# Optimization experiments

Measured on AMD Instinct MI355X. Metric: run time of the kernel, lower is better.

## Reference

```python
import jax, jax.numpy as jnp
import numpy as np

BASE = 64
EOS = 0
PAD = BASE + 1      # 65
BOS = BASE + 2      # 66
VOCAB = BASE + 3    # 67 (use_bos=True)
NACT = BASE + 1     # 65
H = 512
MAX_LEN = 20
BATCH = 32768


def setup_inputs() -> dict:
    key = jax.random.key(0)
    ks = jax.random.split(key, 12)
    s = 1.0 / np.sqrt(H)  # torch-like init scale, avoids gate saturation
    emb = jax.random.normal(ks[1], (VOCAB, H), jnp.float32) * s
    emb = emb.at[PAD].set(0.0)  # padding_idx row is zero in nn.Embedding
    return {
        'encoded': jax.random.normal(ks[0], (BATCH, H), jnp.float32),
        'emb': emb,
        'W_ih': jax.random.normal(ks[2], (4 * H, H), jnp.float32) * s,
        'W_hh': jax.random.normal(ks[3], (4 * H, H), jnp.float32) * s,
        'b_ih': jax.random.normal(ks[4], (4 * H,), jnp.float32) * s,
        'b_hh': jax.random.normal(ks[5], (4 * H,), jnp.float32) * s,
        'Wc': jax.random.normal(ks[6], (H, H), jnp.float32) * s,
        'bc': jax.random.normal(ks[7], (H,), jnp.float32) * s,
        'Wh': jax.random.normal(ks[8], (H, H), jnp.float32) * s,
        'bh': jax.random.normal(ks[9], (H,), jnp.float32) * s,
        'Wa': jax.random.normal(ks[10], (NACT, H), jnp.float32) * s,
        'ba': jax.random.normal(ks[11], (NACT,), jnp.float32) * s,
    }


def _decode(encoded, emb, W_ih, W_hh, b_ih, b_hh, Wc, bc, Wh, bh, Wa, ba):
    B = encoded.shape[0]
    # NOTE: original passes (cell, hidden) to nn.LSTM, which reads it as (h0, c0).
    h0 = encoded @ Wc.T + bc  # cell_proj output -> used as h0
    c0 = encoded @ Wh.T + bh  # hidden_proj output -> used as c0
    last0 = jnp.full((B,), BOS, jnp.int32)
    stopped0 = jnp.zeros((B,), bool)

    def step(carry, _):
        h, c, last, stopped = carry
        x = emb[last]                                   # [B, H]
        gates = x @ W_ih.T + b_ih + h @ W_hh.T + b_hh   # [B, 4H]
        i, f, g, o = jnp.split(gates, 4, axis=-1)
        c = jax.nn.sigmoid(f) * c + jax.nn.sigmoid(i) * jnp.tanh(g)
        h = jax.nn.sigmoid(o) * jnp.tanh(c)
        logits = h @ Wa.T + ba                          # [B, NACT]
        logp = jax.nn.log_softmax(logits, axis=-1)
        action = jnp.argmax(logits, axis=-1).astype(jnp.int32)  # eval-mode greedy
        alive = (~stopped).astype(logits.dtype)
        ent = -jnp.sum(jnp.exp(logp) * logp, axis=-1) * alive
        lp = jnp.take_along_axis(logp, action[:, None], axis=-1)[:, 0] * alive
        action = jnp.where(stopped, PAD, action)
        stopped = stopped | (action == EOS)
        return (h, c, action, stopped), (action, lp, ent)

    _, (msg, lps, ents) = jax.lax.scan(step, (h0, c0, last0, stopped0), None, length=MAX_LEN)
    message = msg.T                                   # [B, L]
    log_probs = lps.T                                 # [B, L]
    entropy_steps = ents.T                            # [B, L]
    message_len = jnp.sum(message != PAD, axis=1, keepdims=True)  # [B, 1]
    entropy = jnp.sum(entropy_steps, axis=1, keepdims=True) / message_len.astype(entropy_steps.dtype)
    return entropy, log_probs, message, message_len


def reference(encoded, emb, W_ih, W_hh, b_ih, b_hh, Wc, bc, Wh, bh, Wa, ba):
    return _decode(encoded, emb, W_ih, W_hh, b_ih, b_hh, Wc, bc, Wh, bh, Wa, ba)
```

## Files before the change

kernel.cpp:

```cpp
#include <hip/hip_runtime.h>
#include <cmath>


#define HH      512
#define G4      2048
#define NACTS   65
#define NVOCAB  67
#define MAXLEN  20
#define NB      32768
#define TM      16
#define NTH     256
#define EOS_TOK 0
#define PAD_TOK 65
#define BOS_TOK 66
#define HSTR    516

__global__ void prep_gxa_kernel(const float* __restrict__ emb,
                                const float* __restrict__ W_ih,
                                const float* __restrict__ b_ih,
                                const float* __restrict__ b_hh,
                                float* __restrict__ gxa4) {
  int id = blockIdx.x * blockDim.x + threadIdx.x;
  if (id >= NVOCAB * G4) return;
  int a = id / G4, rem = id - a * G4;
  int t = rem >> 2, gate = rem & 3;
  int c = gate * HH + t;
  const float* e = emb + (size_t)a * HH;
  const float* w = W_ih + (size_t)c * HH;
  float acc = 0.f;
  for (int k = 0; k < HH; ++k) acc = fmaf(e[k], w[k], acc);
  gxa4[id] = acc + b_ih[c] + b_hh[c];
}

__global__ void prep_w4_kernel(const float* __restrict__ src,
                               float* __restrict__ dst, int cols) {
  int id = blockIdx.x * blockDim.x + threadIdx.x;
  if (id >= cols * HH) return;
  int k4 = id / (cols * 4);
  int rem = id - k4 * cols * 4;
  int c = rem >> 2, j = rem & 3;
  dst[id] = src[(size_t)c * HH + k4 * 4 + j];
}

__global__ void ws_sentinel_kernel(float* out) {
  out[threadIdx.x] = 123000.f;
}

#define FMA4(acc, h, wv) \
  acc = fmaf((h).x, (wv).x, fmaf((h).y, (wv).y, fmaf((h).z, (wv).z, fmaf((h).w, (wv).w, (acc)))))

__global__ __launch_bounds__(NTH, 2)
void decode_kernel(const float* __restrict__ encoded,
                   const float* __restrict__ gxa4,
                   const float* __restrict__ whh4,
                   const float* __restrict__ wc4,
                   const float* __restrict__ wh4,
                   const float* __restrict__ bc,
                   const float* __restrict__ bh,
                   const float* __restrict__ Wa,
                   const float* __restrict__ ba,
                   float* __restrict__ out) {
  __shared__ float sh_h[TM][HSTR];
  __shared__ float sh_wa[16][HSTR];
  __shared__ float sh_logits[TM][NACTS + 3];
  __shared__ int   sh_last[TM];
  __shared__ int   sh_stop[TM];
  __shared__ float sh_ent[TM];
  __shared__ int   sh_len[TM];

  const int t = threadIdx.x;
  const int row0 = blockIdx.x * TM;

  #pragma unroll
  for (int i = 0; i < (TM * HH / 4) / NTH; ++i) {
    int f4 = i * NTH + t;
    int idx = f4 * 4;
    int r = idx >> 9;
    int c = idx & (HH - 1);
    *reinterpret_cast<float4*>(&sh_h[r][c]) =
        *reinterpret_cast<const float4*>(encoded + (size_t)(row0 + r) * HH + c);
  }
  if (t < TM) { sh_last[t] = BOS_TOK; sh_stop[t] = 0; sh_ent[t] = 0.f; sh_len[t] = 0; }
  __syncthreads();

  float hacc[2][TM], cacc[2][TM];
  #pragma unroll
  for (int j = 0; j < 2; ++j)
    #pragma unroll
    for (int r = 0; r < TM; ++r) { hacc[j][r] = 0.f; cacc[j][r] = 0.f; }
  #pragma unroll 1
  for (int k4 = 0; k4 < HH / 4; ++k4) {
    const float* wcb = wc4 + ((size_t)k4 * HH + t) * 4;
    const float* whb = wh4 + ((size_t)k4 * HH + t) * 4;
    float4 wc0 = *reinterpret_cast<const float4*>(wcb);
    float4 wc1 = *reinterpret_cast<const float4*>(wcb + 1024);
    float4 wh0 = *reinterpret_cast<const float4*>(whb);
    float4 wh1 = *reinterpret_cast<const float4*>(whb + 1024);
    #pragma unroll
    for (int r = 0; r < TM; ++r) {
      float4 e = *reinterpret_cast<const float4*>(&sh_h[r][k4 * 4]);
      FMA4(hacc[0][r], e, wc0);
      FMA4(hacc[1][r], e, wc1);
      FMA4(cacc[0][r], e, wh0);
      FMA4(cacc[1][r], e, wh1);
    }
  }
  __syncthreads();
  float cst[2][TM];
  {
    float bc0 = bc[t], bc1 = bc[t + 256];
    float bh0 = bh[t], bh1 = bh[t + 256];
    #pragma unroll
    for (int r = 0; r < TM; ++r) {
      sh_h[r][t] = hacc[0][r] + bc0;
      sh_h[r][t + 256] = hacc[1][r] + bc1;
      cst[0][r] = cacc[0][r] + bh0;
      cst[1][r] = cacc[1][r] + bh1;
    }
  }
  __syncthreads();

  for (int step = 0; step < MAXLEN; ++step) {
    float ai[2][TM], af[2][TM], ag[2][TM], ao[2][TM];
    #pragma unroll
    for (int r = 0; r < TM; ++r) {
      const float* g0 = gxa4 + ((size_t)sh_last[r] * HH + t) * 4;
      float4 ga = *reinterpret_cast<const float4*>(g0);
      float4 gb = *reinterpret_cast<const float4*>(g0 + 1024);
      ai[0][r] = ga.x; af[0][r] = ga.y; ag[0][r] = ga.z; ao[0][r] = ga.w;
      ai[1][r] = gb.x; af[1][r] = gb.y; ag[1][r] = gb.z; ao[1][r] = gb.w;
    }
    #pragma unroll 1
    for (int k4 = 0; k4 < HH / 4; ++k4) {
      const float* wb = whh4 + (size_t)k4 * (G4 * 4) + t * 4;
      float4 wi0 = *reinterpret_cast<const float4*>(wb);
      float4 wf0 = *reinterpret_cast<const float4*>(wb + 2048);
      float4 wg0 = *reinterpret_cast<const float4*>(wb + 4096);
      float4 wo0 = *reinterpret_cast<const float4*>(wb + 6144);
      float4 wi1 = *reinterpret_cast<const float4*>(wb + 1024);
      float4 wf1 = *reinterpret_cast<const float4*>(wb + 2048 + 1024);
      float4 wg1 = *reinterpret_cast<const float4*>(wb + 4096 + 1024);
      float4 wo1 = *reinterpret_cast<const float4*>(wb + 6144 + 1024);
      #pragma unroll
      for (int r = 0; r < TM; ++r) {
        float4 h4 = *reinterpret_cast<const float4*>(&sh_h[r][k4 * 4]);
        FMA4(ai[0][r], h4, wi0);
        FMA4(af[0][r], h4, wf0);
        FMA4(ag[0][r], h4, wg0);
        FMA4(ao[0][r], h4, wo0);
        FMA4(ai[1][r], h4, wi1);
        FMA4(af[1][r], h4, wf1);
        FMA4(ag[1][r], h4, wg1);
        FMA4(ao[1][r], h4, wo1);
      }
    }
    __syncthreads();

    #pragma unroll
    for (int j = 0; j < 2; ++j) {
      int col = t + j * 256;
      #pragma unroll
      for (int r = 0; r < TM; ++r) {
        float iv = 1.f / (1.f + expf(-ai[j][r]));
        float fv = 1.f / (1.f + expf(-af[j][r]));
        float gv = tanhf(ag[j][r]);
        float ov = 1.f / (1.f + expf(-ao[j][r]));
        float cn = fmaf(fv, cst[j][r], iv * gv);
        cst[j][r] = cn;
        sh_h[r][col] = ov * tanhf(cn);
      }
    }
    __syncthreads();

    const int r_lg = t >> 4;
    const int a_lg = t & 15;
    for (int ab = 0; ab < 5; ++ab) {
      int a0 = ab * 16;
      int arows = (a0 + 16 <= NACTS) ? 16 : (NACTS - a0);
      int total4 = arows * HH / 4;
      for (int f4 = t; f4 < total4; f4 += NTH) {
        int idx = f4 * 4;
        int rr = idx >> 9;
        int cc = idx & (HH - 1);
        *reinterpret_cast<float4*>(&sh_wa[rr][cc]) =
            *reinterpret_cast<const float4*>(Wa + (size_t)(a0 + rr) * HH + cc);
      }
      __syncthreads();
      if (a_lg < arows) {
        float acc = 0.f;
        #pragma unroll 1
        for (int k4 = 0; k4 < HH / 4; ++k4) {
          float4 h4 = *reinterpret_cast<const float4*>(&sh_h[r_lg][k4 * 4]);
          float4 w4 = *reinterpret_cast<const float4*>(&sh_wa[a_lg][k4 * 4]);
          FMA4(acc, h4, w4);
        }
        sh_logits[r_lg][a0 + a_lg] = acc + ba[a0 + a_lg];
      }
      __syncthreads();
    }

    if (t < TM) {
      const int r = t;
      float m = sh_logits[r][0];
      int am = 0;
      #pragma unroll 1
      for (int a = 1; a < NACTS; ++a) {
        float v = sh_logits[r][a];
        if (v > m) { m = v; am = a; }
      }
      float s = 0.f;
      #pragma unroll 1
      for (int a = 0; a < NACTS; ++a) s += expf(sh_logits[r][a] - m);
      float logZ = m + logf(s);
      float pl = 0.f;
      #pragma unroll 1
      for (int a = 0; a < NACTS; ++a) {
        float l = sh_logits[r][a];
        pl = fmaf(expf(l - logZ), l, pl);
      }
      float ent = logZ - pl;
      int stopped = sh_stop[r];
      float lp   = stopped ? 0.f : (sh_logits[r][am] - logZ);
      float entc = stopped ? 0.f : ent;
      int act = stopped ? PAD_TOK : am;
      int grow = row0 + r;
      out[NB + (size_t)grow * MAXLEN + step] = lp;
      out[NB + (size_t)NB * MAXLEN + (size_t)grow * MAXLEN + step] = (float)act;
      sh_ent[r] += entc;
      if (act != PAD_TOK) sh_len[r] += 1;
      if (act == EOS_TOK) sh_stop[r] = 1;
      sh_last[r] = act;
    }
    __syncthreads();
  }

  if (t < TM) {
    int r = t, grow = row0 + r;
    float lenf = (float)sh_len[r];
    out[grow] = sh_ent[r] / lenf;
    out[NB + 2 * (size_t)NB * MAXLEN + grow] = lenf;
  }
}

extern "C" void kernel_launch(void* const* d_in, const int* in_sizes, int n_in,
                              void* d_out, int out_size, void* d_ws, size_t ws_size,
                              hipStream_t stream) {
  const float* encoded = (const float*)d_in[0];
  const float* emb     = (const float*)d_in[1];
  const float* W_ih    = (const float*)d_in[2];
  const float* W_hh    = (const float*)d_in[3];
  const float* b_ih    = (const float*)d_in[4];
  const float* b_hh    = (const float*)d_in[5];
  const float* Wc      = (const float*)d_in[6];
  const float* bc      = (const float*)d_in[7];
  const float* Wh      = (const float*)d_in[8];
  const float* bh      = (const float*)d_in[9];
  const float* Wa      = (const float*)d_in[10];
  const float* ba      = (const float*)d_in[11];
  float* out = (float*)d_out;

  size_t need = ((size_t)NVOCAB * G4 + (size_t)G4 * HH + 2 * (size_t)HH * HH) * 4;
  if (ws_size < need) {
    ws_sentinel_kernel<<<1, 64, 0, stream>>>(out);
    return;
  }

  float* ws   = (float*)d_ws;
  float* gxa4 = ws;
  float* whh4 = gxa4 + NVOCAB * G4;
  float* wc4  = whh4 + (size_t)HH * G4;
  float* wh4  = wc4 + (size_t)HH * HH;

  prep_gxa_kernel<<<(NVOCAB * G4 + 255) / 256, 256, 0, stream>>>(emb, W_ih, b_ih, b_hh, gxa4);
  prep_w4_kernel<<<(G4 * HH + 255) / 256, 256, 0, stream>>>(W_hh, whh4, G4);
  prep_w4_kernel<<<(HH * HH + 255) / 256, 256, 0, stream>>>(Wc, wc4, HH);
  prep_w4_kernel<<<(HH * HH + 255) / 256, 256, 0, stream>>>(Wh, wh4, HH);

  decode_kernel<<<NB / TM, NTH, 0, stream>>>(encoded, gxa4, whh4, wc4, wh4,
                                             bc, bh, Wa, ba, out);
}
```

Before: 21.04 ms.

## Read action-head weights from a padded interleaved global layout instead of staging through LDS

```diff
diff --git a/kernel.cpp b/kernel.cpp
--- a/kernel.cpp
+++ b/kernel.cpp
@@ -5,6 +5,7 @@
 #define HH      512
 #define G4      2048
 #define NACTS   65
+#define NAP     80
 #define NVOCAB  67
 #define MAXLEN  20
 #define NB      32768
@@ -42,6 +43,16 @@
   dst[id] = src[(size_t)c * HH + k4 * 4 + j];
 }
 
+__global__ void prep_wa4_kernel(const float* __restrict__ Wa,
+                                float* __restrict__ dst) {
+  int id = blockIdx.x * blockDim.x + threadIdx.x;
+  if (id >= (HH / 4) * NAP * 4) return;
+  int k4 = id / (NAP * 4);
+  int rem = id - k4 * NAP * 4;
+  int a = rem >> 2, j = rem & 3;
+  dst[id] = (a < NACTS) ? Wa[(size_t)a * HH + k4 * 4 + j] : 0.f;
+}
+
 __global__ void ws_sentinel_kernel(float* out) {
   out[threadIdx.x] = 123000.f;
 }
@@ -49,7 +60,7 @@
 #define FMA4(acc, h, wv) \
   acc = fmaf((h).x, (wv).x, fmaf((h).y, (wv).y, fmaf((h).z, (wv).z, fmaf((h).w, (wv).w, (acc)))))
 
-__global__ __launch_bounds__(NTH, 2)
+__global__ __launch_bounds__(NTH, 1)
 void decode_kernel(const float* __restrict__ encoded,
                    const float* __restrict__ gxa4,
                    const float* __restrict__ whh4,
@@ -57,11 +68,10 @@
                    const float* __restrict__ wh4,
                    const float* __restrict__ bc,
                    const float* __restrict__ bh,
-                   const float* __restrict__ Wa,
+                   const float* __restrict__ wa4,
                    const float* __restrict__ ba,
                    float* __restrict__ out) {
   __shared__ float sh_h[TM][HSTR];
-  __shared__ float sh_wa[16][HSTR];
   __shared__ float sh_logits[TM][NACTS + 3];
   __shared__ int   sh_last[TM];
   __shared__ int   sh_stop[TM];
@@ -172,32 +182,23 @@
     }
     __syncthreads();
 
-    const int r_lg = t >> 4;
-    const int a_lg = t & 15;
-    for (int ab = 0; ab < 5; ++ab) {
-      int a0 = ab * 16;
-      int arows = (a0 + 16 <= NACTS) ? 16 : (NACTS - a0);
-      int total4 = arows * HH / 4;
-      for (int f4 = t; f4 < total4; f4 += NTH) {
-        int idx = f4 * 4;
-        int rr = idx >> 9;
-        int cc = idx & (HH - 1);
-        *reinterpret_cast<float4*>(&sh_wa[rr][cc]) =
-            *reinterpret_cast<const float4*>(Wa + (size_t)(a0 + rr) * HH + cc);
-      }
-      __syncthreads();
-      if (a_lg < arows) {
+    {
+      const int r_lg = t >> 4;
+      const int a_lg = t & 15;
+      #pragma unroll 1
+      for (int ab = 0; ab < 5; ++ab) {
+        int a = ab * 16 + a_lg;
         float acc = 0.f;
-        #pragma unroll 1
+        #pragma unroll 4
         for (int k4 = 0; k4 < HH / 4; ++k4) {
           float4 h4 = *reinterpret_cast<const float4*>(&sh_h[r_lg][k4 * 4]);
-          float4 w4 = *reinterpret_cast<const float4*>(&sh_wa[a_lg][k4 * 4]);
+          float4 w4 = *reinterpret_cast<const float4*>(wa4 + ((size_t)k4 * NAP + a) * 4);
           FMA4(acc, h4, w4);
         }
-        sh_logits[r_lg][a0 + a_lg] = acc + ba[a0 + a_lg];
-      }
-      __syncthreads();
-    }
+        if (a < NACTS) sh_logits[r_lg][a] = acc + ba[a];
+      }
+    }
+    __syncthreads();
 
     if (t < TM) {
       const int r = t;
@@ -259,7 +260,8 @@
   const float* ba      = (const float*)d_in[11];
   float* out = (float*)d_out;
 
-  size_t need = ((size_t)NVOCAB * G4 + (size_t)G4 * HH + 2 * (size_t)HH * HH) * 4;
+  size_t need = ((size_t)NVOCAB * G4 + (size_t)G4 * HH + 2 * (size_t)HH * HH
+                 + (size_t)(HH / 4) * NAP * 4) * 4;
   if (ws_size < need) {
     ws_sentinel_kernel<<<1, 64, 0, stream>>>(out);
     return;
@@ -270,12 +272,14 @@
   float* whh4 = gxa4 + NVOCAB * G4;
   float* wc4  = whh4 + (size_t)HH * G4;
   float* wh4  = wc4 + (size_t)HH * HH;
+  float* wa4  = wh4 + (size_t)HH * HH;
 
   prep_gxa_kernel<<<(NVOCAB * G4 + 255) / 256, 256, 0, stream>>>(emb, W_ih, b_ih, b_hh, gxa4);
   prep_w4_kernel<<<(G4 * HH + 255) / 256, 256, 0, stream>>>(W_hh, whh4, G4);
   prep_w4_kernel<<<(HH * HH + 255) / 256, 256, 0, stream>>>(Wc, wc4, HH);
   prep_w4_kernel<<<(HH * HH + 255) / 256, 256, 0, stream>>>(Wh, wh4, HH);
+  prep_wa4_kernel<<<((HH / 4) * NAP * 4 + 255) / 256, 256, 0, stream>>>(Wa, wa4);
 
   decode_kernel<<<NB / TM, NTH, 0, stream>>>(encoded, gxa4, whh4, wc4, wh4,
-                                             bc, bh, Wa, ba, out);
-}
+                                             bc, bh, wa4, ba, out);
+}
```

Result: slower. 34.66 ms (+64.7%).
